# Optimization experiments

Hardware: AMD Instinct MI355X
Metric: run time of the kernel (lower is better)

Reference implementation:

```python
import jax, jax.numpy as jnp
import numpy as np

N_NODES = 100000
N_EDGES = 1600000
IN_F = 64
HID_F = 64
HID_CH = 32
OUT_F = 16


def setup_inputs() -> dict:
    key = jax.random.key(0)
    ks = jax.random.split(key, 12)
    feat = jax.random.normal(ks[0], (N_NODES, IN_F), dtype=jnp.float32)
    edge_src = jax.random.randint(ks[1], (N_EDGES,), 0, N_NODES, dtype=jnp.int32)
    edge_dst = jax.random.randint(ks[2], (N_EDGES,), 0, N_NODES, dtype=jnp.int32)
    s = 1.414 / np.sqrt(IN_F)
    fc1_w = jax.random.normal(ks[3], (HID_F, IN_F), dtype=jnp.float32) * s
    fc1_b = jnp.zeros((HID_F,), dtype=jnp.float32)
    filt_w = jax.random.normal(ks[4], (HID_F, IN_F), dtype=jnp.float32) * s
    filt_b = jnp.zeros((HID_F,), dtype=jnp.float32)
    att_w1 = jax.random.normal(ks[5], (HID_F, HID_CH), dtype=jnp.float32) * (1.0 / np.sqrt(HID_F))
    att_b1 = jnp.zeros((HID_CH,), dtype=jnp.float32)
    att_w2 = jax.random.normal(ks[6], (HID_CH, 1), dtype=jnp.float32) * (1.0 / np.sqrt(HID_CH))
    fc2_w = jax.random.normal(ks[7], (OUT_F, HID_F), dtype=jnp.float32) * (1.414 / np.sqrt(HID_F))
    fc2_b = jnp.zeros((OUT_F,), dtype=jnp.float32)
    return {
        "feat": feat, "edge_src": edge_src, "edge_dst": edge_dst,
        "fc1_w": fc1_w, "fc1_b": fc1_b, "filt_w": filt_w, "filt_b": filt_b,
        "att_w1": att_w1, "att_b1": att_b1, "att_w2": att_w2,
        "fc2_w": fc2_w, "fc2_b": fc2_b,
    }


def _lp_filter(feat, edge_src, edge_dst, filt_w, filt_b):
    # Low-pass (GCN-style) filter: symmetric-normalized neighborhood aggregation
    # of the linearly transformed features.  x: [N, H]
    x = feat @ filt_w.T + filt_b
    ones = jnp.ones((edge_src.shape[0],), dtype=x.dtype)
    deg_out = jax.ops.segment_sum(ones, edge_src, num_segments=N_NODES)
    deg_in = jax.ops.segment_sum(ones, edge_dst, num_segments=N_NODES)
    inv_sqrt_out = jax.lax.rsqrt(jnp.maximum(deg_out, 1.0))
    inv_sqrt_in = jax.lax.rsqrt(jnp.maximum(deg_in, 1.0))
    # gather-transform-scatter: msg_e = x[src_e] * norm_e  ->  sum at dst
    coef = inv_sqrt_out[edge_src] * inv_sqrt_in[edge_dst]  # [E]
    msg = x[edge_src] * coef[:, None]                       # [E, H]
    return jax.ops.segment_sum(msg, edge_dst, num_segments=N_NODES)  # [N, H]


def _channel_attention(z, att_w1, att_b1, att_w2):
    # z: [N, C, H]; semantic (channel) attention a la HAN
    w = jnp.tanh(z @ att_w1 + att_b1) @ att_w2        # [N, C, 1]
    beta = jax.nn.softmax(w.mean(axis=0), axis=0)     # [C, 1]
    return (beta[None, :, :] * z).sum(axis=1)         # [N, H]


def reference(feat, edge_src, edge_dst, fc1_w, fc1_b, filt_w, filt_b,
              att_w1, att_b1, att_w2, fc2_w, fc2_b):
    h1 = jnp.tanh(feat @ fc1_w.T + fc1_b)                          # MLP branch [N, H]
    h2 = _lp_filter(feat, edge_src, edge_dst, filt_w, filt_b)      # graph branch [N, H]
    z = jnp.stack([h1, h2], axis=1)                                # [N, 2, H]
    fused = _channel_attention(z, att_w1, att_b1, att_w2)          # [N, H]
    return fused @ fc2_w.T + fc2_b                                 # [N, OUT_F]
```

## Files before the change

### kernel.cpp

```cpp
#include <hip/hip_runtime.h>
#include <math.h>

#define N_NODESC 100000
#define N_EDGESC 1600000
#define NBUCK 1563
#define BSLACK 1280
#define SCHUNK 4096
#define NSBLK 391

__device__ __forceinline__ float fast_tanh(float x) {
    float ax = fabsf(x);
    float e = __expf(-2.f * ax);
    float r = (1.f - e) * __builtin_amdgcn_rcpf(1.f + e);
    return copysignf(r, x);
}

__global__ void binit_kernel(int* __restrict__ bcur, int* __restrict__ sbcur) {
    int i = blockIdx.x * blockDim.x + threadIdx.x;
    if (i < NBUCK) { bcur[i] = i * BSLACK; sbcur[i] = i * BSLACK; }
}

__global__ __launch_bounds__(1024) void scatter_dual_kernel(
    const int* __restrict__ src, const int* __restrict__ dst,
    int* __restrict__ bcur, int* __restrict__ sbcur,
    unsigned* __restrict__ bedges, unsigned char* __restrict__ sbytes) {
    __shared__ int histd[NBUCK];
    __shared__ int hists[NBUCK];
    int tid = threadIdx.x;
    int e_beg = blockIdx.x * SCHUNK;
    int e_end = min(e_beg + SCHUNK, N_EDGESC);
    for (int i = tid; i < NBUCK; i += 1024) { histd[i] = 0; hists[i] = 0; }
    __syncthreads();

    int ss[4], dd[4];
    int cnt = 0;
    for (int i = e_beg + tid; i < e_end; i += 1024) {
        ss[cnt] = src[i];
        dd[cnt] = dst[i];
        cnt++;
    }
#pragma unroll
    for (int j = 0; j < 4; j++) {
        if (j < cnt) {
            atomicAdd(&histd[dd[j] >> 6], 1);
            atomicAdd(&hists[ss[j] >> 6], 1);
        }
    }
    __syncthreads();
    for (int i = tid; i < NBUCK; i += 1024) {
        int c = histd[i];
        if (c > 0) histd[i] = atomicAdd(&bcur[i], c);
        int c2 = hists[i];
        if (c2 > 0) hists[i] = atomicAdd(&sbcur[i], c2);
    }
    __syncthreads();
#pragma unroll
    for (int j = 0; j < 4; j++) {
        if (j < cnt) {
            int slot = atomicAdd(&histd[dd[j] >> 6], 1);
            bedges[slot] = (unsigned)ss[j] | ((unsigned)(dd[j] & 63) << 17);
            int slot2 = atomicAdd(&hists[ss[j] >> 6], 1);
            sbytes[slot2] = (unsigned char)(ss[j] & 63);
        }
    }
}

__global__ __launch_bounds__(256) void gemm_kernel(
    const float* __restrict__ feat,
    const float* __restrict__ w1, const float* __restrict__ b1,
    const float* __restrict__ w2, const float* __restrict__ b2,
    const int* __restrict__ sbcur, const unsigned char* __restrict__ sbytes,
    float* __restrict__ h1, float* __restrict__ xs) {
    __shared__ float sf[128 * 68];
    __shared__ int ldeg[128];
    int tid = threadIdx.x;
    int base = blockIdx.x * 128;
    if (tid < 128) ldeg[tid] = 0;
    for (int k = 0; k < 8; k++) {
        int fi = tid + k * 256;
        int node = fi >> 4, f4 = fi & 15;
        float4 v = make_float4(0.f, 0.f, 0.f, 0.f);
        if (base + node < N_NODESC)
            v = ((const float4*)feat)[(size_t)(base + node) * 16 + f4];
        float* d = &sf[node * 68 + f4 * 4];
        d[0] = v.x; d[1] = v.y; d[2] = v.z; d[3] = v.w;
    }
    __syncthreads();

#pragma unroll
    for (int h = 0; h < 2; h++) {
        int sb = blockIdx.x * 2 + h;
        if (sb < NBUCK) {
            int sbeg = sb * BSLACK;
            int sm = sbcur[sb] - sbeg;
            for (int i = tid; i < sm; i += 256)
                atomicAdd(&ldeg[h * 64 + (int)sbytes[sbeg + i]], 1);
        }
    }

    int lane = tid & 63;
    int og = __builtin_amdgcn_readfirstlane(tid >> 6);
    const float* wp1 = w1 + og * 16 * 64;
    const float* wp2 = w2 + og * 16 * 64;

    float a1[2][16], a2[2][16];
#pragma unroll
    for (int o = 0; o < 16; o++) {
        float bb1 = b1[og * 16 + o], bb2 = b2[og * 16 + o];
        a1[0][o] = bb1; a1[1][o] = bb1;
        a2[0][o] = bb2; a2[1][o] = bb2;
    }

    for (int fq = 0; fq < 16; fq++) {
        float4 fv0 = *(const float4*)&sf[lane * 68 + fq * 4];
        float4 fv1 = *(const float4*)&sf[(lane + 64) * 68 + fq * 4];
#pragma unroll
        for (int o = 0; o < 16; o++) {
            float4 wv1 = *(const float4*)&wp1[o * 64 + fq * 4];
            float4 wv2 = *(const float4*)&wp2[o * 64 + fq * 4];
            a1[0][o] += fv0.x * wv1.x + fv0.y * wv1.y + fv0.z * wv1.z + fv0.w * wv1.w;
            a1[1][o] += fv1.x * wv1.x + fv1.y * wv1.y + fv1.z * wv1.z + fv1.w * wv1.w;
            a2[0][o] += fv0.x * wv2.x + fv0.y * wv2.y + fv0.z * wv2.z + fv0.w * wv2.w;
            a2[1][o] += fv1.x * wv2.x + fv1.y * wv2.y + fv1.z * wv2.z + fv1.w * wv2.w;
        }
    }

    __syncthreads();

#pragma unroll
    for (int j = 0; j < 2; j++) {
        int g = base + lane + j * 64;
        if (g >= N_NODESC) continue;
        float is = rsqrtf(fmaxf((float)ldeg[j * 64 + lane], 1.f));
#pragma unroll
        for (int oq = 0; oq < 4; oq++) {
            float4 t, u;
            t.x = fast_tanh(a1[j][oq * 4 + 0]); t.y = fast_tanh(a1[j][oq * 4 + 1]);
            t.z = fast_tanh(a1[j][oq * 4 + 2]); t.w = fast_tanh(a1[j][oq * 4 + 3]);
            u.x = a2[j][oq * 4 + 0] * is;   u.y = a2[j][oq * 4 + 1] * is;
            u.z = a2[j][oq * 4 + 2] * is;   u.w = a2[j][oq * 4 + 3] * is;
            ((float4*)h1)[(size_t)g * 16 + og * 4 + oq] = t;
            ((float4*)xs)[(size_t)g * 16 + og * 4 + oq] = u;
        }
    }
}

__global__ __launch_bounds__(256) void agg4_kernel(const int* __restrict__ bcur,
                                                   const unsigned* __restrict__ bedges,
                                                   const float* __restrict__ xs,
                                                   float* __restrict__ h2) {
    __shared__ unsigned eraw[BSLACK];
    __shared__ unsigned eled[BSLACK];
    __shared__ int loff[65];
    __shared__ int lcnt[64];
    __shared__ int lcur[64];
    int tid = threadIdx.x, lane = tid & 63, wid = tid >> 6;
    int b = blockIdx.x;
    int beg = b * BSLACK;
    int m = bcur[b] - beg;

    if (tid < 64) lcnt[tid] = 0;
    __syncthreads();
    for (int i = tid; i < m; i += 256) {
        unsigned pk = bedges[beg + i];
        eraw[i] = pk;
        atomicAdd(&lcnt[pk >> 17], 1);
    }
    __syncthreads();
    if (wid == 0) {
        int c = lcnt[lane];
        int v = c;
#pragma unroll
        for (int off = 1; off < 64; off <<= 1) {
            int t = __shfl_up(v, off, 64);
            if (lane >= off) v += t;
        }
        loff[lane] = v - c;
        lcur[lane] = v - c;
        if (lane == 63) loff[64] = v;
    }
    __syncthreads();
    for (int i = tid; i < m; i += 256) {
        unsigned pk = eraw[i];
        int pos = atomicAdd(&lcur[pk >> 17], 1);
        eled[pos] = pk & 0x1FFFFu;
    }
    __syncthreads();

    int nbase = b * 64;
#pragma unroll 1
    for (int t = 0; t < 16; t++) {
        int nl = wid * 16 + t;
        int s0 = loff[nl], s1 = loff[nl + 1];
        float acc = 0.f;
        for (int k = s0; k < s1; k += 16) {
            int cnt = s1 - k; if (cnt > 16) cnt = 16;
            unsigned sv = eled[min(k + (lane & 15), s1 - 1)];
            float v[16];
#pragma unroll
            for (int j = 0; j < 16; j++) {
                if (j < cnt) {
                    int sj = __shfl((int)sv, j, 64);
                    v[j] = xs[(size_t)sj * 64 + lane];
                }
            }
#pragma unroll
            for (int j = 0; j < 16; j++)
                if (j < cnt) acc += v[j];
        }
        int g = nbase + nl;
        if (g < N_NODESC) {
            float isq = rsqrtf(fmaxf((float)(s1 - s0), 1.f));
            h2[(size_t)g * 64 + lane] = acc * isq;
        }
    }
}

__global__ __launch_bounds__(256) void attb_kernel(const float* __restrict__ H,
                                                   const float* __restrict__ aw1,
                                                   const float* __restrict__ ab1,
                                                   const float* __restrict__ aw2,
                                                   float* __restrict__ wslot) {
    __shared__ float sf[128 * 68];
    __shared__ float ssc[4][128];
    int tid = threadIdx.x;
    int lane = tid & 63;
    int og = __builtin_amdgcn_readfirstlane(tid >> 6);
    int base = blockIdx.x * 128;

    for (int k = 0; k < 8; k++) {
        int fi = tid + k * 256;
        int node = fi >> 4, f4 = fi & 15;
        float4 v = make_float4(0.f, 0.f, 0.f, 0.f);
        if (base + node < N_NODESC)
            v = ((const float4*)H)[(size_t)(base + node) * 16 + f4];
        float* d = &sf[node * 68 + f4 * 4];
        d[0] = v.x; d[1] = v.y; d[2] = v.z; d[3] = v.w;
    }
    __syncthreads();

    float acc[2][8];
#pragma unroll
    for (int c = 0; c < 8; c++) {
        float bb = ab1[og * 8 + c];
        acc[0][c] = bb; acc[1][c] = bb;
    }
    for (int fq = 0; fq < 16; fq++) {
        float4 fv0 = *(const float4*)&sf[lane * 68 + fq * 4];
        float4 fv1 = *(const float4*)&sf[(lane + 64) * 68 + fq * 4];
#pragma unroll
        for (int c = 0; c < 8; c++) {
            float w0 = aw1[(fq * 4 + 0) * 32 + og * 8 + c];
            float w1 = aw1[(fq * 4 + 1) * 32 + og * 8 + c];
            float w2 = aw1[(fq * 4 + 2) * 32 + og * 8 + c];
            float w3 = aw1[(fq * 4 + 3) * 32 + og * 8 + c];
            acc[0][c] += fv0.x * w0 + fv0.y * w1 + fv0.z * w2 + fv0.w * w3;
            acc[1][c] += fv1.x * w0 + fv1.y * w1 + fv1.z * w2 + fv1.w * w3;
        }
    }
    float s0 = 0.f, s1 = 0.f;
#pragma unroll
    for (int c = 0; c < 8; c++) {
        float w2c = aw2[og * 8 + c];
        s0 += fast_tanh(acc[0][c]) * w2c;
        s1 += fast_tanh(acc[1][c]) * w2c;
    }
    ssc[og][lane] = s0;
    ssc[og][lane + 64] = s1;
    __syncthreads();

    float v = 0.f;
    if (tid < 128) {
        v = ssc[0][tid] + ssc[1][tid] + ssc[2][tid] + ssc[3][tid];
        if (base + tid >= N_NODESC) v = 0.f;
    }
#pragma unroll
    for (int off = 32; off; off >>= 1) v += __shfl_down(v, off, 64);
    if (lane == 0) atomicAdd(wslot, v);
}

__global__ void beta_kernel(const float* __restrict__ wsum, float* __restrict__ beta) {
    float w0 = wsum[0] / (float)N_NODESC, w1 = wsum[1] / (float)N_NODESC;
    float m = fmaxf(w0, w1);
    float e0 = expf(w0 - m), e1 = expf(w1 - m);
    float inv = 1.f / (e0 + e1);
    beta[0] = e0 * inv;
    beta[1] = e1 * inv;
}

__global__ __launch_bounds__(256) void out_kernel(const float* __restrict__ h1,
                                                  const float* __restrict__ h2,
                                                  const float* __restrict__ beta,
                                                  const float* __restrict__ w,
                                                  const float* __restrict__ b,
                                                  float* __restrict__ out) {
    __shared__ float sw[16 * 68];
    int tid = threadIdx.x;
    {
        int o = tid >> 4, f4 = tid & 15;
        float4 v = ((const float4*)w)[tid];
        float* d = &sw[o * 68 + f4 * 4];
        d[0] = v.x; d[1] = v.y; d[2] = v.z; d[3] = v.w;
    }
    __syncthreads();
    int o = tid & 15, ln = tid >> 4;
    int node = blockIdx.x * 16 + ln;
    if (node >= N_NODESC) return;
    float b0 = beta[0], b1v = beta[1];
    const float4* r1 = (const float4*)(h1 + (size_t)node * 64);
    const float4* r2 = (const float4*)(h2 + (size_t)node * 64);
    float acc = b[o];
    for (int fq = 0; fq < 16; fq++) {
        float4 x1 = r1[fq], x2 = r2[fq];
        float4 wv = *(const float4*)&sw[o * 68 + fq * 4];
        acc += (b0 * x1.x + b1v * x2.x) * wv.x + (b0 * x1.y + b1v * x2.y) * wv.y
             + (b0 * x1.z + b1v * x2.z) * wv.z + (b0 * x1.w + b1v * x2.w) * wv.w;
    }
    out[(size_t)node * 16 + o] = acc;
}

extern "C" void kernel_launch(void* const* d_in, const int* in_sizes, int n_in,
                              void* d_out, int out_size, void* d_ws, size_t ws_size,
                              hipStream_t stream) {
    (void)in_sizes; (void)n_in; (void)out_size; (void)ws_size;
    const float* feat = (const float*)d_in[0];
    const int*   esrc = (const int*)d_in[1];
    const int*   edst = (const int*)d_in[2];
    const float* fc1w = (const float*)d_in[3];
    const float* fc1b = (const float*)d_in[4];
    const float* fltw = (const float*)d_in[5];
    const float* fltb = (const float*)d_in[6];
    const float* aw1  = (const float*)d_in[7];
    const float* ab1  = (const float*)d_in[8];
    const float* aw2  = (const float*)d_in[9];
    const float* fc2w = (const float*)d_in[10];
    const float* fc2b = (const float*)d_in[11];
    float* out = (float*)d_out;

    char* ws = (char*)d_ws;
    size_t off = 0;
    auto alloc = [&](size_t bytes) {
        char* p = ws + off;
        off += (bytes + 255) & ~(size_t)255;
        return p;
    };
    float*         h1     = (float*)alloc((size_t)N_NODESC * 64 * 4);
    float*         xs     = (float*)alloc((size_t)N_NODESC * 64 * 4);
    float*         h2     = (float*)alloc((size_t)N_NODESC * 64 * 4);
    int*           bcur   = (int*)alloc((size_t)NBUCK * 4);
    int*           sbcur  = (int*)alloc((size_t)NBUCK * 4);
    unsigned*      bedges = (unsigned*)alloc((size_t)NBUCK * BSLACK * 4);
    unsigned char* sbytes = (unsigned char*)alloc((size_t)NBUCK * BSLACK);
    float*         wsum   = (float*)alloc(16 * 4);
    float*         beta   = (float*)alloc(16 * 4);

    hipMemsetAsync(wsum, 0, 2 * 4, stream);

    binit_kernel<<<(NBUCK + 255) / 256, 256, 0, stream>>>(bcur, sbcur);
    scatter_dual_kernel<<<NSBLK, 1024, 0, stream>>>(esrc, edst, bcur, sbcur,
                                                    bedges, sbytes);
    gemm_kernel<<<(N_NODESC + 127) / 128, 256, 0, stream>>>(
        feat, fc1w, fc1b, fltw, fltb, sbcur, sbytes, h1, xs);
    agg4_kernel<<<NBUCK, 256, 0, stream>>>(bcur, bedges, xs, h2);
    attb_kernel<<<(N_NODESC + 127) / 128, 256, 0, stream>>>(h1, aw1, ab1, aw2, &wsum[0]);
    attb_kernel<<<(N_NODESC + 127) / 128, 256, 0, stream>>>(h2, aw1, ab1, aw2, &wsum[1]);
    beta_kernel<<<1, 1, 0, stream>>>(wsum, beta);
    out_kernel<<<(N_NODESC + 15) / 16, 256, 0, stream>>>(h1, h2, beta, fc2w, fc2b, out);
}
```

Measured before the change: 357.0 us.

## Fuse aggregation, attention, softmax and output into one cooperative persistent kernel

Replaces the agg4, two attb, beta and out launches with a single cooperative persistent kernel that uses grid.sync between phases. The h1 attention tiles are interleaved with edge aggregation in the first phase, so independent work shares the grid. Attention tiles shrink to 64 nodes so the work list maps onto NBUCK items. The intent is to remove launch gaps and tail effects, at the cost of grid-wide barriers and a grid capped by occupancy, which may reduce latency hiding for the gather-heavy aggregation.

```diff
diff --git a/kernel.cpp b/kernel.cpp
--- a/kernel.cpp
+++ b/kernel.cpp
@@ -1,5 +1,8 @@
 #include <hip/hip_runtime.h>
+#include <hip/hip_cooperative_groups.h>
 #include <math.h>
+
+namespace cg = cooperative_groups;
 
 #define N_NODESC 100000
 #define N_EDGESC 1600000
@@ -7,6 +10,7 @@
 #define BSLACK 1280
 #define SCHUNK 4096
 #define NSBLK 391
+#define NCHUNK 6250
 
 __device__ __forceinline__ float fast_tanh(float x) {
     float ax = fabsf(x);
@@ -145,17 +149,18 @@
     }
 }
 
-__global__ __launch_bounds__(256) void agg4_kernel(const int* __restrict__ bcur,
-                                                   const unsigned* __restrict__ bedges,
-                                                   const float* __restrict__ xs,
-                                                   float* __restrict__ h2) {
-    __shared__ unsigned eraw[BSLACK];
-    __shared__ unsigned eled[BSLACK];
-    __shared__ int loff[65];
-    __shared__ int lcnt[64];
-    __shared__ int lcur[64];
+#define SMEM_BYTES 18688
+
+__device__ void agg_bucket(int b, const int* __restrict__ bcur,
+                           const unsigned* __restrict__ bedges,
+                           const float* __restrict__ xs,
+                           float* __restrict__ h2, char* smem) {
+    unsigned* eraw = (unsigned*)smem;
+    unsigned* eled = (unsigned*)(smem + 5120);
+    int* loff = (int*)(smem + 10240);
+    int* lcnt = (int*)(smem + 10504);
+    int* lcur = (int*)(smem + 10760);
     int tid = threadIdx.x, lane = tid & 63, wid = tid >> 6;
-    int b = blockIdx.x;
     int beg = b * BSLACK;
     int m = bcur[b] - beg;
 
@@ -214,21 +219,21 @@
             h2[(size_t)g * 64 + lane] = acc * isq;
         }
     }
-}
-
-__global__ __launch_bounds__(256) void attb_kernel(const float* __restrict__ H,
-                                                   const float* __restrict__ aw1,
-                                                   const float* __restrict__ ab1,
-                                                   const float* __restrict__ aw2,
-                                                   float* __restrict__ wslot) {
-    __shared__ float sf[128 * 68];
-    __shared__ float ssc[4][128];
-    int tid = threadIdx.x;
-    int lane = tid & 63;
+    __syncthreads();
+}
+
+__device__ void att_tile(const float* __restrict__ H, int tile,
+                         const float* __restrict__ aw1,
+                         const float* __restrict__ ab1,
+                         const float* __restrict__ aw2,
+                         float* __restrict__ wslot, char* smem) {
+    float* sf  = (float*)smem;
+    float* ssc = (float*)(smem + 17408);
+    int tid = threadIdx.x, lane = tid & 63;
     int og = __builtin_amdgcn_readfirstlane(tid >> 6);
-    int base = blockIdx.x * 128;
-
-    for (int k = 0; k < 8; k++) {
+    int base = tile * 64;
+
+    for (int k = 0; k < 4; k++) {
         int fi = tid + k * 256;
         int node = fi >> 4, f4 = fi & 15;
         float4 v = make_float4(0.f, 0.f, 0.f, 0.f);
@@ -239,44 +244,108 @@
     }
     __syncthreads();
 
-    float acc[2][8];
-#pragma unroll
-    for (int c = 0; c < 8; c++) {
-        float bb = ab1[og * 8 + c];
-        acc[0][c] = bb; acc[1][c] = bb;
-    }
+    float acc[8];
+#pragma unroll
+    for (int c = 0; c < 8; c++) acc[c] = ab1[og * 8 + c];
     for (int fq = 0; fq < 16; fq++) {
-        float4 fv0 = *(const float4*)&sf[lane * 68 + fq * 4];
-        float4 fv1 = *(const float4*)&sf[(lane + 64) * 68 + fq * 4];
+        float4 fv = *(const float4*)&sf[lane * 68 + fq * 4];
 #pragma unroll
         for (int c = 0; c < 8; c++) {
-            float w0 = aw1[(fq * 4 + 0) * 32 + og * 8 + c];
-            float w1 = aw1[(fq * 4 + 1) * 32 + og * 8 + c];
-            float w2 = aw1[(fq * 4 + 2) * 32 + og * 8 + c];
-            float w3 = aw1[(fq * 4 + 3) * 32 + og * 8 + c];
-            acc[0][c] += fv0.x * w0 + fv0.y * w1 + fv0.z * w2 + fv0.w * w3;
-            acc[1][c] += fv1.x * w0 + fv1.y * w1 + fv1.z * w2 + fv1.w * w3;
-        }
-    }
-    float s0 = 0.f, s1 = 0.f;
-#pragma unroll
-    for (int c = 0; c < 8; c++) {
-        float w2c = aw2[og * 8 + c];
-        s0 += fast_tanh(acc[0][c]) * w2c;
-        s1 += fast_tanh(acc[1][c]) * w2c;
-    }
-    ssc[og][lane] = s0;
-    ssc[og][lane + 64] = s1;
-    __syncthreads();
-
-    float v = 0.f;
-    if (tid < 128) {
-        v = ssc[0][tid] + ssc[1][tid] + ssc[2][tid] + ssc[3][tid];
+            acc[c] += fv.x * aw1[(fq * 4 + 0) * 32 + og * 8 + c]
+                    + fv.y * aw1[(fq * 4 + 1) * 32 + og * 8 + c]
+                    + fv.z * aw1[(fq * 4 + 2) * 32 + og * 8 + c]
+                    + fv.w * aw1[(fq * 4 + 3) * 32 + og * 8 + c];
+        }
+    }
+    float s = 0.f;
+#pragma unroll
+    for (int c = 0; c < 8; c++) s += fast_tanh(acc[c]) * aw2[og * 8 + c];
+    ssc[og * 64 + lane] = s;
+    __syncthreads();
+
+    if (tid < 64) {
+        float v = ssc[tid] + ssc[64 + tid] + ssc[128 + tid] + ssc[192 + tid];
         if (base + tid >= N_NODESC) v = 0.f;
-    }
-#pragma unroll
-    for (int off = 32; off; off >>= 1) v += __shfl_down(v, off, 64);
-    if (lane == 0) atomicAdd(wslot, v);
+#pragma unroll
+        for (int off = 32; off; off >>= 1) v += __shfl_down(v, off, 64);
+        if (tid == 0) atomicAdd(wslot, v);
+    }
+    __syncthreads();
+}
+
+__global__ __launch_bounds__(256) void mega_kernel(
+    const int* __restrict__ bcur, const unsigned* __restrict__ bedges,
+    const float* __restrict__ xs, float* __restrict__ h2,
+    const float* __restrict__ h1,
+    const float* __restrict__ aw1, const float* __restrict__ ab1,
+    const float* __restrict__ aw2, float* __restrict__ wsum,
+    const float* __restrict__ fc2w, const float* __restrict__ fc2b,
+    float* __restrict__ out) {
+    cg::grid_group grid = cg::this_grid();
+    __shared__ __align__(16) char smem[SMEM_BYTES];
+    int nb = gridDim.x;
+    int tid = threadIdx.x;
+
+    for (int it = blockIdx.x; it < 2 * NBUCK; it += nb) {
+        if (it < NBUCK) agg_bucket(it, bcur, bedges, xs, h2, smem);
+        else           att_tile(h1, it - NBUCK, aw1, ab1, aw2, &wsum[0], smem);
+    }
+    __threadfence();
+    grid.sync();
+
+    for (int it = blockIdx.x; it < NBUCK; it += nb)
+        att_tile(h2, it, aw1, ab1, aw2, &wsum[1], smem);
+    __threadfence();
+    grid.sync();
+
+    float w0 = wsum[0] * (1.f / (float)N_NODESC);
+    float w1 = wsum[1] * (1.f / (float)N_NODESC);
+    float mx = fmaxf(w0, w1);
+    float e0 = __expf(w0 - mx), e1 = __expf(w1 - mx);
+    float inv = 1.f / (e0 + e1);
+    float b0 = e0 * inv, b1v = e1 * inv;
+
+    float* sw = (float*)smem;
+    {
+        int o = tid >> 4, f4 = tid & 15;
+        float4 v = ((const float4*)fc2w)[tid];
+        float* d = &sw[o * 68 + f4 * 4];
+        d[0] = v.x; d[1] = v.y; d[2] = v.z; d[3] = v.w;
+    }
+    __syncthreads();
+    int o = tid & 15, ln = tid >> 4;
+    float bb = fc2b[o];
+    for (int chunk = blockIdx.x; chunk < NCHUNK; chunk += nb) {
+        int node = chunk * 16 + ln;
+        if (node >= N_NODESC) continue;
+        const float4* r1 = (const float4*)(h1 + (size_t)node * 64);
+        const float4* r2 = (const float4*)(h2 + (size_t)node * 64);
+        float acc = bb;
+        for (int fq = 0; fq < 16; fq++) {
+            float4 x1 = r1[fq], x2 = r2[fq];
+            float4 wv = *(const float4*)&sw[o * 68 + fq * 4];
+            acc += (b0 * x1.x + b1v * x2.x) * wv.x + (b0 * x1.y + b1v * x2.y) * wv.y
+                 + (b0 * x1.z + b1v * x2.z) * wv.z + (b0 * x1.w + b1v * x2.w) * wv.w;
+        }
+        out[(size_t)node * 16 + o] = acc;
+    }
+}
+
+__global__ __launch_bounds__(256) void agg4_kernel(const int* __restrict__ bcur,
+                                                   const unsigned* __restrict__ bedges,
+                                                   const float* __restrict__ xs,
+                                                   float* __restrict__ h2) {
+    __shared__ __align__(16) char smem[SMEM_BYTES];
+    agg_bucket(blockIdx.x, bcur, bedges, xs, h2, smem);
+}
+
+__global__ __launch_bounds__(256) void attb_kernel(const float* __restrict__ H,
+                                                   const float* __restrict__ aw1,
+                                                   const float* __restrict__ ab1,
+                                                   const float* __restrict__ aw2,
+                                                   float* __restrict__ wslot) {
+    __shared__ __align__(16) char smem[SMEM_BYTES];
+    att_tile(H, blockIdx.x, aw1, ab1, aw2, wslot, smem);
 }
 
 __global__ void beta_kernel(const float* __restrict__ wsum, float* __restrict__ beta) {
@@ -361,9 +430,37 @@
                                                     bedges, sbytes);
     gemm_kernel<<<(N_NODESC + 127) / 128, 256, 0, stream>>>(
         feat, fc1w, fc1b, fltw, fltb, sbcur, sbytes, h1, xs);
-    agg4_kernel<<<NBUCK, 256, 0, stream>>>(bcur, bedges, xs, h2);
-    attb_kernel<<<(N_NODESC + 127) / 128, 256, 0, stream>>>(h1, aw1, ab1, aw2, &wsum[0]);
-    attb_kernel<<<(N_NODESC + 127) / 128, 256, 0, stream>>>(h2, aw1, ab1, aw2, &wsum[1]);
-    beta_kernel<<<1, 1, 0, stream>>>(wsum, beta);
-    out_kernel<<<(N_NODESC + 15) / 16, 256, 0, stream>>>(h1, h2, beta, fc2w, fc2b, out);
-}
+
+    static int mgrid = -1;
+    if (mgrid < 0) {
+        int nbpc = 0;
+        hipError_t oe = hipOccupancyMaxActiveBlocksPerMultiprocessor(
+            &nbpc, mega_kernel, 256, 0);
+        if (oe != hipSuccess || nbpc < 1) { nbpc = 1; (void)hipGetLastError(); }
+        long cap = (long)nbpc * 256;
+        mgrid = (int)(cap < NBUCK ? cap : NBUCK);
+        if (mgrid < 1) mgrid = 1;
+    }
+
+    const int*      a_bcur   = bcur;
+    const unsigned* a_bedges = bedges;
+    const float*    a_xs     = xs;
+    float*          a_h2     = h2;
+    const float*    a_h1     = h1;
+    void* margs[] = { (void*)&a_bcur, (void*)&a_bedges, (void*)&a_xs,
+                      (void*)&a_h2, (void*)&a_h1, (void*)&aw1, (void*)&ab1,
+                      (void*)&aw2, (void*)&wsum, (void*)&fc2w, (void*)&fc2b,
+                      (void*)&out };
+    hipError_t st = hipLaunchCooperativeKernel((const void*)mega_kernel,
+                                               dim3(mgrid), dim3(256),
+                                               margs, 0, stream);
+    if (st != hipSuccess) {
+        (void)hipGetLastError();
+        agg4_kernel<<<NBUCK, 256, 0, stream>>>(bcur, bedges, xs, h2);
+        attb_kernel<<<NBUCK, 256, 0, stream>>>(h1, aw1, ab1, aw2, &wsum[0]);
+        attb_kernel<<<NBUCK, 256, 0, stream>>>(h2, aw1, ab1, aw2, &wsum[1]);
+        beta_kernel<<<1, 1, 0, stream>>>(wsum, beta);
+        out_kernel<<<(N_NODESC + 15) / 16, 256, 0, stream>>>(h1, h2, beta,
+                                                             fc2w, fc2b, out);
+    }
+}
```

New measurement: 547.4 us. 1.53x slower.
